# Kernel tuning notes

Hardware: AMD Instinct MI355X
Metric: run time of the kernel (lower is better)

The kernel has to match this reference:

```python
import jax, jax.numpy as jnp
import numpy as np

BATCH = 1_000_000
NUM_BINS = 37  # num_classes == 37 -> ranges [0, 13, 26, 37]
STARTS = jnp.array([0, 13, 26], dtype=jnp.int32)
ENDS = jnp.array([13, 26, 37], dtype=jnp.int32)
NEG_INF = jnp.float32(-1e30)
LOG_CLAMP = -100.0  # torch BCE clamps log terms at -100


def setup_inputs() -> dict:
    key = jax.random.key(0)
    k1, k2, k3 = jax.random.split(key, 3)
    preds = jax.random.normal(k1, (BATCH, NUM_BINS), dtype=jnp.float32)
    labels = jax.random.normal(k2, (BATCH, NUM_BINS), dtype=jnp.float32)
    obj_classes = jax.random.randint(k3, (BATCH,), 0, 3, dtype=jnp.int32)
    weights = jnp.ones((3,), dtype=jnp.float32)
    return {"preds": preds, "labels": labels, "weights": weights,
            "obj_classes": obj_classes}


def reference(preds, labels, weights, obj_classes):
    # Per-sample ragged slice [start, end) expressed as a mask over the 37 bins.
    idx = jnp.arange(NUM_BINS)
    s = STARTS[obj_classes][:, None]  # (B, 1)
    e = ENDS[obj_classes][:, None]    # (B, 1)
    mask = (idx >= s) & (idx < e)     # (B, 37)

    # Softmax restricted to the active slice (masked positions -> -inf logits).
    logp = jax.nn.log_softmax(jnp.where(mask, preds, NEG_INF), axis=-1)
    p = jnp.exp(logp)
    t = jax.nn.softmax(jnp.where(mask, labels, NEG_INF), axis=-1)

    # BCE(p, t) summed over the slice (size_average=False):
    # -(t*log p + (1-t)*log(1-p)), with torch-style log clamping at -100.
    logp_c = jnp.maximum(logp, LOG_CLAMP)
    log1mp = jnp.maximum(jnp.log1p(-p), LOG_CLAMP)
    bce = jnp.where(mask, -(t * logp_c + (1.0 - t) * log1mp), 0.0)

    per_sample = bce.sum(axis=-1) * weights[obj_classes]  # (B,)
    losses = jax.ops.segment_sum(per_sample, obj_classes, num_segments=3)
    total = losses.sum() / jnp.float32(preds.shape[0])
    return (total[None], losses[0][None], losses[1][None], losses[2][None])
```

## Files before the change

kernel.cpp:

```cpp
#include <hip/hip_runtime.h>

constexpr int BATCH = 1000000;
constexpr int NBINS = 37;
constexpr int TPB = 256;
constexpr int TILE_ROWS = 256;
constexpr int TILE_FLOATS = TILE_ROWS * NBINS;
constexpr int NV_FULL = TILE_FLOATS / 4;
constexpr float NEG_BIG = -1e30f;
constexpr float LOGCLAMP = -100.0f;

__global__ __launch_bounds__(TPB, 4)
void adviser_loss_kernel(const float* __restrict__ preds,
                         const float* __restrict__ labels,
                         const float* __restrict__ weights,
                         const int* __restrict__ obj_classes,
                         float* __restrict__ out)
{
    __shared__ float tile[TILE_FLOATS];
    __shared__ float cls_sum[3];

    const int tid   = threadIdx.x;
    const int row0  = blockIdx.x * TILE_ROWS;
    const int nrows = min(TILE_ROWS, BATCH - row0);
    const bool full = (nrows == TILE_ROWS);
    const int nvec  = (nrows * NBINS) >> 2;

    if (tid < 3) cls_sum[tid] = 0.0f;

    const int   crow = min(row0 + tid, BATCH - 1);
    const int   c    = obj_classes[crow];
    const float w    = weights[c];

    const float4* gp = (const float4*)(preds + (size_t)row0 * NBINS);
    if (full) {
        #pragma unroll
        for (int k = 0; k < 10; ++k) {
            const int i = tid + k * TPB;
            if (i < NV_FULL)
                __builtin_amdgcn_global_load_lds(
                    (const __attribute__((address_space(1))) void*)(gp + i),
                    (__attribute__((address_space(3))) void*)(&tile[i * 4]),
                    16, 0, 0);
        }
    } else {
        for (int i = tid; i < nvec; i += TPB)
            ((float4*)tile)[i] = gp[i];
    }

    const float4* gl = (const float4*)(labels + (size_t)row0 * NBINS);
    float4 lv4[10];
    #pragma unroll
    for (int k = 0; k < 10; ++k) {
        const int i = tid + k * TPB;
        if (i < nvec) lv4[k] = gl[i];
    }

    __syncthreads();

    const bool valid = (tid < nrows);
    const int  s     = 13 * c;
    const int  L     = (c == 2) ? 11 : 13;
    const int  base  = tid * NBINS + s;

    float pv[13], ep[13];
    #pragma unroll
    for (int j = 0; j < 13; ++j)
        pv[j] = (j < L) ? tile[base + j] : NEG_BIG;
    float Z = 0.0f;
    #pragma unroll
    for (int j = 0; j < 13; ++j) { ep[j] = __expf(pv[j]); Z += ep[j]; }

    __syncthreads();

    #pragma unroll
    for (int k = 0; k < 10; ++k) {
        const int i = tid + k * TPB;
        if (i < nvec) ((float4*)tile)[i] = lv4[k];
    }
    __syncthreads();

    float et[13];
    float Zt = 0.0f;
    #pragma unroll
    for (int j = 0; j < 13; ++j) {
        const float lv = (j < L) ? tile[base + j] : NEG_BIG;
        et[j] = __expf(lv);
        Zt += et[j];
    }

    const float logZ  = __logf(Z);
    const float rcpZ  = __builtin_amdgcn_rcpf(Z);
    const float rcpZt = __builtin_amdgcn_rcpf(Zt);

    float acc = 0.0f;
    #pragma unroll
    for (int j = 0; j < 13; ++j) {
        const float logp = pv[j] - logZ;
        const float p    = ep[j] * rcpZ;
        const float ca   = fmaxf(logp, LOGCLAMP);
        const float cb   = fmaxf(__logf(fmaxf(1.0f - p, 0.0f)), LOGCLAMP);
        const float t    = et[j] * rcpZt;
        acc += cb + t * (ca - cb);
    }
    const float per_sample = valid ? (-acc) * w : 0.0f;

    float v0 = (c == 0) ? per_sample : 0.0f;
    float v1 = (c == 1) ? per_sample : 0.0f;
    float v2 = (c == 2) ? per_sample : 0.0f;
    #pragma unroll
    for (int off = 32; off > 0; off >>= 1) {
        v0 += __shfl_down(v0, off, 64);
        v1 += __shfl_down(v1, off, 64);
        v2 += __shfl_down(v2, off, 64);
    }
    if ((tid & 63) == 0) {
        atomicAdd(&cls_sum[0], v0);
        atomicAdd(&cls_sum[1], v1);
        atomicAdd(&cls_sum[2], v2);
    }
    __syncthreads();
    if (tid < 3) atomicAdd(&out[1 + tid], cls_sum[tid]);
    if (tid == 0)
        atomicAdd(&out[0], (cls_sum[0] + cls_sum[1] + cls_sum[2]) * (1.0f / (float)BATCH));
}

extern "C" void kernel_launch(void* const* d_in, const int* in_sizes, int n_in,
                              void* d_out, int out_size, void* d_ws, size_t ws_size,
                              hipStream_t stream) {
    const float* preds   = (const float*)d_in[0];
    const float* labels  = (const float*)d_in[1];
    const float* weights = (const float*)d_in[2];
    const int*   obj     = (const int*)d_in[3];
    float* out = (float*)d_out;

    hipMemsetAsync(out, 0, (size_t)out_size * sizeof(float), stream);
    const int grid = (BATCH + TILE_ROWS - 1) / TILE_ROWS;
    adviser_loss_kernel<<<grid, TPB, 0, stream>>>(preds, labels, weights, obj, out);
}
```

Before: 373.6 us.

## Use persistent blocks with double-buffered async LDS prefetch of preds and labels

Result: faster. 331.7 us (-11.2%).

```diff
diff --git a/kernel.cpp b/kernel.cpp
--- a/kernel.cpp
+++ b/kernel.cpp
@@ -1,127 +1,152 @@
 #include <hip/hip_runtime.h>
 
-constexpr int BATCH = 1000000;
-constexpr int NBINS = 37;
-constexpr int TPB = 256;
-constexpr int TILE_ROWS = 256;
-constexpr int TILE_FLOATS = TILE_ROWS * NBINS;
-constexpr int NV_FULL = TILE_FLOATS / 4;
-constexpr float NEG_BIG = -1e30f;
+constexpr int BATCH  = 1000000;
+constexpr int NBINS  = 37;
+constexpr int TPB    = 128;
+constexpr int ROWS   = 128;
+constexpr int TFLOAT = ROWS * NBINS;
+constexpr int TVEC   = TFLOAT / 4;
+constexpr int KFULL  = TVEC / TPB;
+constexpr int VREM   = TVEC - KFULL*TPB;
+constexpr int NTILES = (BATCH + ROWS - 1) / ROWS;
+constexpr int NBLK   = 512;
+constexpr int QT     = NTILES / NBLK;
+constexpr int RT     = NTILES % NBLK;
+constexpr float NEG_BIG  = -1e30f;
 constexpr float LOGCLAMP = -100.0f;
 
-__global__ __launch_bounds__(TPB, 4)
+__global__ __launch_bounds__(TPB, 1)
 void adviser_loss_kernel(const float* __restrict__ preds,
                          const float* __restrict__ labels,
                          const float* __restrict__ weights,
-                         const int* __restrict__ obj_classes,
+                         const int* __restrict__ obj,
                          float* __restrict__ out)
 {
-    __shared__ float tile[TILE_FLOATS];
+    __shared__ float buf[2][2][TFLOAT];
     __shared__ float cls_sum[3];
 
-    const int tid   = threadIdx.x;
-    const int row0  = blockIdx.x * TILE_ROWS;
-    const int nrows = min(TILE_ROWS, BATCH - row0);
-    const bool full = (nrows == TILE_ROWS);
-    const int nvec  = (nrows * NBINS) >> 2;
-
+    const int tid = threadIdx.x;
+    const int b   = blockIdx.x;
     if (tid < 3) cls_sum[tid] = 0.0f;
 
-    const int   crow = min(row0 + tid, BATCH - 1);
-    const int   c    = obj_classes[crow];
-    const float w    = weights[c];
+    const int cnt = QT + (b < RT ? 1 : 0);
+    const int t0  = b * QT + min(b, RT);
 
-    const float4* gp = (const float4*)(preds + (size_t)row0 * NBINS);
-    if (full) {
-        #pragma unroll
-        for (int k = 0; k < 10; ++k) {
-            const int i = tid + k * TPB;
-            if (i < NV_FULL)
+    const float w0 = weights[0], w1 = weights[1], w2 = weights[2];
+
+    auto stage = [&](int sel, int t) {
+        const int rowbase = t * ROWS;
+        const int nrows   = min(ROWS, BATCH - rowbase);
+        const float4* gp = (const float4*)(preds  + (size_t)rowbase * NBINS);
+        const float4* gl = (const float4*)(labels + (size_t)rowbase * NBINS);
+        if (nrows == ROWS) {
+            #pragma unroll
+            for (int k = 0; k < KFULL; ++k) {
+                const int i = tid + k * TPB;
                 __builtin_amdgcn_global_load_lds(
                     (const __attribute__((address_space(1))) void*)(gp + i),
-                    (__attribute__((address_space(3))) void*)(&tile[i * 4]),
+                    (__attribute__((address_space(3))) void*)(&buf[sel][0][i * 4]),
                     16, 0, 0);
+                __builtin_amdgcn_global_load_lds(
+                    (const __attribute__((address_space(1))) void*)(gl + i),
+                    (__attribute__((address_space(3))) void*)(&buf[sel][1][i * 4]),
+                    16, 0, 0);
+            }
+            if (tid < VREM) {
+                const int i = KFULL * TPB + tid;
+                ((float4*)buf[sel][0])[i] = gp[i];
+                ((float4*)buf[sel][1])[i] = gl[i];
+            }
+        } else {
+            const int nv = (nrows * NBINS) >> 2;
+            for (int i = tid; i < nv; i += TPB) {
+                ((float4*)buf[sel][0])[i] = gp[i];
+                ((float4*)buf[sel][1])[i] = gl[i];
+            }
         }
-    } else {
-        for (int i = tid; i < nvec; i += TPB)
-            ((float4*)tile)[i] = gp[i];
+    };
+
+    stage(0, t0);
+    int ccur = obj[min(t0 * ROWS + tid, BATCH - 1)];
+    __syncthreads();
+
+    float a0 = 0.0f, a1 = 0.0f, a2 = 0.0f;
+    int cur = 0;
+
+    for (int ti = 0; ti < cnt; ++ti) {
+        const int t       = t0 + ti;
+        const int rowbase = t * ROWS;
+        const int nrows   = min(ROWS, BATCH - rowbase);
+
+        int cnext = ccur;
+        if (ti + 1 < cnt) {
+            stage(cur ^ 1, t + 1);
+            cnext = obj[min((t + 1) * ROWS + tid, BATCH - 1)];
+        }
+
+        const bool valid = (tid < nrows);
+        const int   c = ccur;
+        const float w = (c == 0) ? w0 : ((c == 1) ? w1 : w2);
+        const int   s = 13 * c;
+        const int   L = (c == 2) ? 11 : 13;
+        const int   base = tid * NBINS + s;
+
+        const float* P = buf[cur][0];
+        const float* T = buf[cur][1];
+
+        float pv[13], ep[13], et[13];
+        float Z = 0.0f, Zt = 0.0f;
+        #pragma unroll
+        for (int j = 0; j < 13; ++j) {
+            const float x = (j < L) ? P[base + j] : NEG_BIG;
+            const float y = (j < L) ? T[base + j] : NEG_BIG;
+            pv[j] = x;
+            ep[j] = __expf(x);  Z  += ep[j];
+            et[j] = __expf(y);  Zt += et[j];
+        }
+        const float logZ  = __logf(Z);
+        const float rcpZ  = __builtin_amdgcn_rcpf(Z);
+        const float rcpZt = __builtin_amdgcn_rcpf(Zt);
+
+        float acc = 0.0f;
+        #pragma unroll
+        for (int j = 0; j < 13; ++j) {
+            const float logp = pv[j] - logZ;
+            const float p    = ep[j] * rcpZ;
+            const float ca   = fmaxf(logp, LOGCLAMP);
+            const float cb   = fmaxf(__logf(fmaxf(1.0f - p, 0.0f)), LOGCLAMP);
+            const float t_   = et[j] * rcpZt;
+            acc += cb + t_ * (ca - cb);
+        }
+        const float per = valid ? (-acc) * w : 0.0f;
+        a0 += (c == 0) ? per : 0.0f;
+        a1 += (c == 1) ? per : 0.0f;
+        a2 += (c == 2) ? per : 0.0f;
+
+        __syncthreads();
+        cur ^= 1;
+        ccur = cnext;
     }
 
-    const float4* gl = (const float4*)(labels + (size_t)row0 * NBINS);
-    float4 lv4[10];
     #pragma unroll
-    for (int k = 0; k < 10; ++k) {
-        const int i = tid + k * TPB;
-        if (i < nvec) lv4[k] = gl[i];
+    for (int off = 32; off > 0; off >>= 1) {
+        a0 += __shfl_down(a0, off, 64);
+        a1 += __shfl_down(a1, off, 64);
+        a2 += __shfl_down(a2, off, 64);
     }
-
-    __syncthreads();
-
-    const bool valid = (tid < nrows);
-    const int  s     = 13 * c;
-    const int  L     = (c == 2) ? 11 : 13;
-    const int  base  = tid * NBINS + s;
-
-    float pv[13], ep[13];
-    #pragma unroll
-    for (int j = 0; j < 13; ++j)
-        pv[j] = (j < L) ? tile[base + j] : NEG_BIG;
-    float Z = 0.0f;
-    #pragma unroll
-    for (int j = 0; j < 13; ++j) { ep[j] = __expf(pv[j]); Z += ep[j]; }
-
-    __syncthreads();
-
-    #pragma unroll
-    for (int k = 0; k < 10; ++k) {
-        const int i = tid + k * TPB;
-        if (i < nvec) ((float4*)tile)[i] = lv4[k];
+    if ((tid & 63) == 0) {
+        atomicAdd(&cls_sum[0], a0);
+        atomicAdd(&cls_sum[1], a1);
+        atomicAdd(&cls_sum[2], a2);
     }
     __syncthreads();
-
-    float et[13];
-    float Zt = 0.0f;
-    #pragma unroll
-    for (int j = 0; j < 13; ++j) {
-        const float lv = (j < L) ? tile[base + j] : NEG_BIG;
-        et[j] = __expf(lv);
-        Zt += et[j];
+    if (tid == 0) {
+        const float s0 = cls_sum[0], s1 = cls_sum[1], s2 = cls_sum[2];
+        atomicAdd(&out[1], s0);
+        atomicAdd(&out[2], s1);
+        atomicAdd(&out[3], s2);
+        atomicAdd(&out[0], (s0 + s1 + s2) * (1.0f / (float)BATCH));
     }
-
-    const float logZ  = __logf(Z);
-    const float rcpZ  = __builtin_amdgcn_rcpf(Z);
-    const float rcpZt = __builtin_amdgcn_rcpf(Zt);
-
-    float acc = 0.0f;
-    #pragma unroll
-    for (int j = 0; j < 13; ++j) {
-        const float logp = pv[j] - logZ;
-        const float p    = ep[j] * rcpZ;
-        const float ca   = fmaxf(logp, LOGCLAMP);
-        const float cb   = fmaxf(__logf(fmaxf(1.0f - p, 0.0f)), LOGCLAMP);
-        const float t    = et[j] * rcpZt;
-        acc += cb + t * (ca - cb);
-    }
-    const float per_sample = valid ? (-acc) * w : 0.0f;
-
-    float v0 = (c == 0) ? per_sample : 0.0f;
-    float v1 = (c == 1) ? per_sample : 0.0f;
-    float v2 = (c == 2) ? per_sample : 0.0f;
-    #pragma unroll
-    for (int off = 32; off > 0; off >>= 1) {
-        v0 += __shfl_down(v0, off, 64);
-        v1 += __shfl_down(v1, off, 64);
-        v2 += __shfl_down(v2, off, 64);
-    }
-    if ((tid & 63) == 0) {
-        atomicAdd(&cls_sum[0], v0);
-        atomicAdd(&cls_sum[1], v1);
-        atomicAdd(&cls_sum[2], v2);
-    }
-    __syncthreads();
-    if (tid < 3) atomicAdd(&out[1 + tid], cls_sum[tid]);
-    if (tid == 0)
-        atomicAdd(&out[0], (cls_sum[0] + cls_sum[1] + cls_sum[2]) * (1.0f / (float)BATCH));
 }
 
 extern "C" void kernel_launch(void* const* d_in, const int* in_sizes, int n_in,
@@ -134,6 +159,5 @@
     float* out = (float*)d_out;
 
     hipMemsetAsync(out, 0, (size_t)out_size * sizeof(float), stream);
-    const int grid = (BATCH + TILE_ROWS - 1) / TILE_ROWS;
-    adviser_loss_kernel<<<grid, TPB, 0, stream>>>(preds, labels, weights, obj, out);
+    adviser_loss_kernel<<<NBLK, TPB, 0, stream>>>(preds, labels, weights, obj, out);
 }
```
